# Optimization experiments

Hardware: AMD Instinct MI355X
Metric: run time of the kernel (lower is better)

Reference implementation:

```python
import jax, jax.numpy as jnp
from jax import lax
import numpy as np

B, T, L = 8, 24, 145
DHID, DFRAME, DEMB, DGCN, V = 1024, 2500, 128, 512, 1024
PF = 300
DINP = DHID + DFRAME + DEMB + DGCN   # 4164 = LSTM input size
DCONT = DHID + DINP                  # 5188 = cont_t size
FLAT = 64 * 7 * 7                    # 3136
BN_EPS = 1e-5
BN_INV = float(1.0 / np.sqrt(1.0 + BN_EPS))  # eval BN with running mean 0, var 1


def setup_inputs() -> dict:
    key = jax.random.key(0)
    ks = iter(jax.random.split(key, 48))
    rn = lambda *s: jax.random.normal(next(ks), s, jnp.float32)
    w = lambda *s: 0.02 * rn(*s)
    return dict(
        enc=rn(B, L, DHID),
        frames=rn(B, T, 512, 7, 7),
        gcn_embedding=rn(B, DGCN),
        h0=jnp.zeros((B, DHID), jnp.float32),
        c0=jnp.zeros((B, DHID), jnp.float32),
        conv1_w=w(256, 512), conv1_b=jnp.zeros((256,), jnp.float32),
        bn1_g=jnp.ones((256,), jnp.float32), bn1_b=jnp.zeros((256,), jnp.float32),
        conv2_w=w(64, 256), conv2_b=jnp.zeros((64,), jnp.float32),
        bn2_g=jnp.ones((64,), jnp.float32), bn2_b=jnp.zeros((64,), jnp.float32),
        fc_w=w(DFRAME, FLAT), fc_b=jnp.zeros((DFRAME,), jnp.float32),
        hfc_w=w(DHID, DHID), hfc_b=jnp.zeros((DHID,), jnp.float32),
        w_ih=w(4 * DHID, DINP), w_hh=w(4 * DHID, DHID),
        b_ih=jnp.zeros((4 * DHID,), jnp.float32), b_hh=jnp.zeros((4 * DHID,), jnp.float32),
        go=0.1 * rn(DEMB),
        emb_w=w(V, DEMB),
        actor_w=w(DEMB, DCONT), actor_b=jnp.zeros((DEMB,), jnp.float32),
        d1_w=w(FLAT, DCONT), d1_b=jnp.zeros((FLAT,), jnp.float32),
        dconv3_w=w(64, 32, 4, 4), dconv3_b=jnp.zeros((32,), jnp.float32),
        bnm2_g=jnp.ones((32,), jnp.float32), bnm2_b=jnp.zeros((32,), jnp.float32),
        dconv2_w=w(32, 16, 4, 4), dconv2_b=jnp.zeros((16,), jnp.float32),
        bnm1_g=jnp.ones((16,), jnp.float32), bnm1_b=jnp.zeros((16,), jnp.float32),
        dconv1_w=w(16, 1, 4, 4), dconv1_b=jnp.zeros((1,), jnp.float32),
    )


def _bn_eval(x, g, b):
    # BatchNorm2d in eval mode with running_mean=0, running_var=1
    return g[None, :, None, None] * (x * BN_INV) + b[None, :, None, None]


def _up2(x):
    # UpsamplingNearest2d(scale_factor=2)
    return jnp.repeat(jnp.repeat(x, 2, axis=2), 2, axis=3)


def _deconv(x, w, b):
    # ConvTranspose2d(k=4, s=2, p=1); torch weight layout (in, out, kH, kW)
    k = jnp.flip(w, (2, 3)).transpose(1, 0, 2, 3)  # -> (out, in, kH, kW)
    y = lax.conv_general_dilated(x, k, window_strides=(1, 1), padding=((2, 2), (2, 2)),
                                 lhs_dilation=(2, 2),
                                 dimension_numbers=('NCHW', 'OIHW', 'NCHW'))
    return y + b[None, :, None, None]


def reference(enc, frames, gcn_embedding, h0, c0,
              conv1_w, conv1_b, bn1_g, bn1_b, conv2_w, conv2_b, bn2_g, bn2_b, fc_w, fc_b,
              hfc_w, hfc_b, w_ih, w_hh, b_ih, b_hh, go, emb_w, actor_w, actor_b,
              d1_w, d1_b, dconv3_w, dconv3_b, bnm2_g, bnm2_b,
              dconv2_w, dconv2_b, bnm1_g, bnm1_b, dconv1_w, dconv1_b):

    def vis_encode(frame):  # [B,512,7,7] -> [B,DFRAME]
        x = jnp.einsum('bchw,oc->bohw', frame, conv1_w) + conv1_b[None, :, None, None]
        x = jax.nn.relu(_bn_eval(x, bn1_g, bn1_b))
        x = jnp.einsum('bchw,oc->bohw', x, conv2_w) + conv2_b[None, :, None, None]
        x = jax.nn.relu(_bn_eval(x, bn2_g, bn2_b))
        return x.reshape(-1, FLAT) @ fc_w.T + fc_b

    def mask_decode(cont):  # [B,DCONT] -> [B,1,300,300]
        x = jax.nn.relu(cont @ d1_w.T + d1_b).reshape(-1, 64, 7, 7)
        x = _deconv(_up2(x), dconv3_w, dconv3_b)          # 14 -> 28
        x = jax.nn.relu(_bn_eval(x, bnm2_g, bnm2_b))
        x = _deconv(_up2(x), dconv2_w, dconv2_b)          # 56 -> 112
        x = jax.nn.relu(_bn_eval(x, bnm1_g, bnm1_b))
        x = _deconv(x, dconv1_w, dconv1_b)                # 112 -> 224
        return jax.image.resize(x, (x.shape[0], 1, PF, PF), method='bilinear')

    def step(carry, frame_t):
        h, c, e_t = carry
        vis = vis_encode(frame_t)
        hq = h @ hfc_w.T + hfc_b
        score = jax.nn.softmax(jnp.einsum('bld,bd->bl', enc, hq), axis=1)  # [B,L]
        weighted = jnp.einsum('bl,bld->bd', score, enc)
        inp = jnp.concatenate([vis, weighted, e_t, gcn_embedding], axis=1)  # [B,DINP]
        gates = inp @ w_ih.T + b_ih + h @ w_hh.T + b_hh
        i, f, g, o = jnp.split(gates, 4, axis=1)
        c_new = jax.nn.sigmoid(f) * c + jax.nn.sigmoid(i) * jnp.tanh(g)
        h_new = jax.nn.sigmoid(o) * jnp.tanh(c_new)
        cont = jnp.concatenate([h_new, inp], axis=1)  # [B,DCONT]
        action = (cont @ actor_w.T + actor_b) @ emb_w.T  # [B,V]
        mask = mask_decode(cont)
        e_new = emb_w[jnp.argmax(action, axis=1)]  # greedy feed-back
        return (h_new, c_new, e_new), (action, mask, score[:, :, None])

    e0 = jnp.tile(go[None, :], (enc.shape[0], 1))
    (h_T, c_T, _), (actions, masks, attns) = lax.scan(
        step, (h0, c0, e0), jnp.swapaxes(frames, 0, 1))
    out_action = jnp.swapaxes(actions, 0, 1)   # [B,T,V]
    out_mask = jnp.swapaxes(masks, 0, 1)       # [B,T,1,300,300]
    out_attn = jnp.swapaxes(attns, 0, 1)       # [B,T,L,1]
    return (out_action, out_mask, out_attn, h_T, c_T)
```

## Files before the change

### kernel.cpp

```cpp
#include <hip/hip_runtime.h>
#include <cstdint>
#include <cstddef>

#define DEV __device__ __forceinline__
typedef short bf16x8 __attribute__((ext_vector_type(8)));
typedef float fl4 __attribute__((ext_vector_type(4)));
typedef float f32x4 __attribute__((ext_vector_type(4)));
typedef unsigned short u16;

#define BN_INV 0.9999950000375f

DEV float b2f(u16 u){ return __uint_as_float(((unsigned)u)<<16); }
DEV u16 f2b(float f){ unsigned u = __float_as_uint(f); unsigned r = (u + 0x7FFFu + ((u>>16)&1u))>>16; return (u16)r; }

DEV bf16x8 load8(const u16* p){ return *(const bf16x8*)p; }
DEV bf16x8 load8(const float* p){
  fl4 a = *(const fl4*)p; fl4 b = *(const fl4*)(p+4);
  bf16x8 r;
  r[0]=(short)f2b(a[0]); r[1]=(short)f2b(a[1]); r[2]=(short)f2b(a[2]); r[3]=(short)f2b(a[3]);
  r[4]=(short)f2b(b[0]); r[5]=(short)f2b(b[1]); r[6]=(short)f2b(b[2]); r[7]=(short)f2b(b[3]);
  return r;
}


__global__ __launch_bounds__(256) void k_pack_frames(const float* __restrict__ fr, u16* __restrict__ XT){
  int bt = blockIdx.x, tid = threadIdx.x;
  for (int e=0;e<128;e++){
    int flat = e*256 + tid;
    int p = flat>>9, c = flat&511;
    u16 v = 0;
    if (p < 49) v = f2b(fr[((size_t)bt*512 + c)*49 + p]);
    XT[((size_t)bt*64 + p)*512 + c] = v;
  }
}

__global__ __launch_bounds__(256) void k_pack_wseq(const float* __restrict__ w_ih, const float* __restrict__ w_hh,
                                                   u16* __restrict__ wseq){
  int r = blockIdx.x, tid = threadIdx.x;
  const float* wr = w_ih + (size_t)r*4164;
  for (int j=tid;j<2176;j+=256){
    float v = (j < 1024) ? w_hh[(size_t)r*1024 + j] : wr[2500 + (j-1024)];
    wseq[(size_t)r*2176 + j] = f2b(v);
  }
}

__global__ __launch_bounds__(256) void k_pack_dseq(const float* __restrict__ d1_w, const float* __restrict__ actor_w,
                                                   u16* __restrict__ dseq){
  int r = blockIdx.x, tid = threadIdx.x;
  const float* wr = (r < 3136) ? (d1_w + (size_t)r*5188) : (actor_w + (size_t)(r-3136)*5188);
  for (int j=tid;j<2176;j+=256){
    float v = (j < 1024) ? wr[j] : wr[3524 + (j-1024)];
    dseq[(size_t)r*2176 + j] = f2b(v);
  }
}

__global__ __launch_bounds__(256) void k_pack_wvg(const float* __restrict__ w_ih, u16* __restrict__ wvg, int rbase){
  int r = rbase + blockIdx.x, tid = threadIdx.x;
  const float* wr = w_ih + (size_t)r*4164;
  u16* dst = wvg + (size_t)blockIdx.x*3072;
  for (int j=tid;j<3072;j+=256){
    float v = 0.f;
    if (j < 2500) v = wr[j];
    else if (j < 3012) v = wr[3652 + (j-2500)];
    dst[j] = f2b(v);
  }
}

__global__ __launch_bounds__(256) void k_pack_dvg(const float* __restrict__ d1_w, const float* __restrict__ actor_w,
                                                  u16* __restrict__ dvg, int rbase){
  int r = rbase + blockIdx.x, tid = threadIdx.x;
  const float* wr = (r < 3136) ? (d1_w + (size_t)r*5188) : (actor_w + (size_t)(r-3136)*5188);
  u16* dst = dvg + (size_t)blockIdx.x*3072;
  for (int j=tid;j<3072;j+=256){
    float v = 0.f;
    if (j < 2500) v = wr[1024 + j];
    else if (j < 3012) v = wr[4676 + (j-2500)];
    dst[j] = f2b(v);
  }
}

__global__ __launch_bounds__(256) void k_hfcT(const float* __restrict__ hfc_w, u16* __restrict__ hfcT){
  int idx = blockIdx.x*256 + threadIdx.x;
  int k = idx>>10, o = idx&1023;
  hfcT[idx] = f2b(hfc_w[o*1024 + k]);
}

DEV u16 wt_map(const float* w, int n, int k, int CIN, int COUT){
  int o = n % COUT; int cls = n / COUT;
  if (cls >= 4) return 0;
  int py = cls>>1, px = cls&1;
  int i = k/9; int dd = k - i*9; int dy = dd/3, dx = dd - dy*3;
  if (i >= CIN) return 0;
  int ky = (py==0) ? (dy==0 ? 3 : (dy==1 ? 1 : -1)) : (dy==1 ? 2 : (dy==2 ? 0 : -1));
  int kx = (px==0) ? (dx==0 ? 3 : (dx==1 ? 1 : -1)) : (dx==1 ? 2 : (dx==2 ? 0 : -1));
  if (ky < 0 || kx < 0) return 0;
  return f2b(w[((i*COUT + o)*4 + ky)*4 + kx]);
}

__global__ __launch_bounds__(256) void k_misc(
  const float* b_ih, const float* b_hh, const float* d1_b, const float* actor_b,
  const float* emb_w, const float* h0, const float* c0,
  const float* dw3, const float* dw2, const float* dw1,
  float* bias_g, float* bias_da, u16* embT, float* hb0, float* cws,
  u16* Wt3, u16* Wt2, u16* Wt1)
{
  int blk = blockIdx.x, tid = threadIdx.x;
  if (blk < 16){ int i = blk*256+tid; if (i<4096) bias_g[i] = b_ih[i] + b_hh[i]; }
  else if (blk < 29){ int i = (blk-16)*256+tid; if (i<3264) bias_da[i] = (i<3136)? d1_b[i] : actor_b[i-3136]; }
  else if (blk < 541){ int i = (blk-29)*256+tid; int j = i>>10, v = i&1023; embT[i] = f2b(emb_w[v*128 + j]); }
  else if (blk < 573){ int i = (blk-541)*256+tid; if (i<8192){ hb0[i] = h0[i]; cws[i] = c0[i]; } }
  else if (blk < 574){ for (int i=tid;i<2560;i+=256){ int n=i/160, k=i-n*160; Wt1[i] = wt_map(dw1,n,k,16,1); } }
  else if (blk < 590){ for (int i=(blk-574)*256+tid; i<18432; i+=16*256){ int n=i/288, k=i-n*288; Wt2[i] = wt_map(dw2,n,k,32,16); } }
  else { for (int i=(blk-590)*256+tid; i<73728; i+=168*256){ int n=i/576, k=i-n*576; Wt3[i] = wt_map(dw3,n,k,64,32); } }
}

__global__ __launch_bounds__(256) void k_eb(const float* __restrict__ enc, const float* __restrict__ hfc_b, float* __restrict__ eb){
  int li = blockIdx.x*4 + (threadIdx.x>>6);
  int lane = threadIdx.x & 63;
  if (li >= 1160) return;
  const float* ep = enc + (size_t)li*1024;
  float a = 0.f;
  for (int k=lane;k<1024;k+=64) a += ep[k]*hfc_b[k];
  #pragma unroll
  for (int off=32; off; off>>=1) a += __shfl_xor(a, off);
  if (lane == 0) eb[li] = a;
}

__global__ __launch_bounds__(256) void k_vis_in(const u16* __restrict__ Y2, u16* __restrict__ vis_in){
  int bt = blockIdx.x, tid = threadIdx.x;
  for (int f=tid; f<3136; f+=256){
    int c = f/49, p = f - c*49;
    vis_in[(size_t)bt*3136 + f] = Y2[((size_t)bt*64 + p)*64 + c];
  }
}

__global__ __launch_bounds__(256) void k_xin(const u16* __restrict__ vis, const float* __restrict__ gcn, u16* __restrict__ xin2){
  int bt = blockIdx.x, tid = threadIdx.x, b = bt/24;
  for (int j=tid;j<3072;j+=256){
    u16 v = 0;
    if (j < 2500) v = vis[(size_t)bt*2500 + j];
    else if (j < 3012) v = f2b(gcn[b*512 + (j-2500)]);
    xin2[(size_t)bt*3072 + j] = v;
  }
}

template<int OUTB, int ACT, typename TA, typename TB>
__global__ __launch_bounds__(256) void gemm64(
  const TA* __restrict__ A, int lda, const TB* __restrict__ Bm, int ldb,
  void* __restrict__ Cv, int ldc, int M, int N, int K,
  const float* __restrict__ bias, const float* __restrict__ cb, const float* __restrict__ gg, const float* __restrict__ bb)
{
  __shared__ u16 sA[64*72];
  __shared__ u16 sB[64*72];
  int tid = threadIdx.x, lane = tid & 63, w = tid >> 6;
  int wm = w & 1, wn = w >> 1;
  int m0 = blockIdx.x*64, n0 = blockIdx.y*64;
  f32x4 acc[2][2];
  #pragma unroll
  for (int a=0;a<2;a++)
    #pragma unroll
    for (int b=0;b<2;b++){ acc[a][b][0]=0;acc[a][b][1]=0;acc[a][b][2]=0;acc[a][b][3]=0; }

  for (int k0=0;k0<K;k0+=64){
    #pragma unroll
    for (int j=0;j<2;j++){
      int c = tid + 256*j; int row = c>>3; int col = (c&7)*8;
      bf16x8 va = {0,0,0,0,0,0,0,0};
      int gm = m0 + row;
      if (gm < M) va = load8(A + (size_t)gm*lda + k0 + col);
      *(bf16x8*)(&sA[row*72 + col]) = va;
      bf16x8 vb = {0,0,0,0,0,0,0,0};
      int gn = n0 + row;
      if (gn < N) vb = load8(Bm + (size_t)gn*ldb + k0 + col);
      *(bf16x8*)(&sB[row*72 + col]) = vb;
    }
    __syncthreads();
    #pragma unroll
    for (int kk=0;kk<2;kk++){
      bf16x8 af[2], bfv[2];
      #pragma unroll
      for (int tm=0;tm<2;tm++) af[tm]  = *(const bf16x8*)(&sA[(wm*32+tm*16+(lane&15))*72 + kk*32 + (lane>>4)*8]);
      #pragma unroll
      for (int tn=0;tn<2;tn++) bfv[tn] = *(const bf16x8*)(&sB[(wn*32+tn*16+(lane&15))*72 + kk*32 + (lane>>4)*8]);
      #pragma unroll
      for (int tm=0;tm<2;tm++)
        #pragma unroll
        for (int tn=0;tn<2;tn++)
          acc[tm][tn] = __builtin_amdgcn_mfma_f32_16x16x32_bf16(af[tm], bfv[tn], acc[tm][tn], 0,0,0);
    }
    __syncthreads();
  }
  int ml = (lane>>4)*4, nl = lane&15;
  #pragma unroll
  for (int tm=0;tm<2;tm++)
    #pragma unroll
    for (int tn=0;tn<2;tn++)
      #pragma unroll
      for (int r=0;r<4;r++){
        int gm = m0 + wm*32 + tm*16 + ml + r;
        int gn = n0 + wn*32 + tn*16 + nl;
        if (gm < M && gn < N){
          float v = acc[tm][tn][r];
          if (ACT == 0){ if (bias) v += bias[gn]; }
          else { v = (v + cb[gn])*BN_INV*gg[gn] + bb[gn]; v = fmaxf(v, 0.f); }
          if (OUTB) ((u16*)Cv)[(size_t)gm*ldc + gn] = f2b(v);
          else      ((float*)Cv)[(size_t)gm*ldc + gn] = v;
        }
      }
}

template<int OUTB, typename TA, typename TB>
__global__ __launch_bounds__(64) void gemm16(
  const TA* __restrict__ A, int lda, const TB* __restrict__ Bm, int ldb,
  void* __restrict__ Cv, int ldc, int M, int N, int K, const float* __restrict__ bias)
{
  int lane = threadIdx.x;
  int m0 = blockIdx.x*16, n0 = blockIdx.y*16;
  int gm = m0 + (lane&15); if (gm > M-1) gm = M-1;
  int gn = n0 + (lane&15); if (gn > N-1) gn = N-1;
  const TA* ap = A  + (size_t)gm*lda + ((lane>>4)*8);
  const TB* bp = Bm + (size_t)gn*ldb + ((lane>>4)*8);
  f32x4 acc = {0,0,0,0};
  #pragma unroll 4
  for (int ks=0; ks<K; ks+=32){
    bf16x8 a = load8(ap + ks);
    bf16x8 b = load8(bp + ks);
    acc = __builtin_amdgcn_mfma_f32_16x16x32_bf16(a, b, acc, 0,0,0);
  }
  int nn = n0 + (lane&15);
  if (nn >= N) return;
  #pragma unroll
  for (int r=0;r<4;r++){
    int mm = m0 + (lane>>4)*4 + r;
    if (mm < M){
      float v = acc[r];
      if (bias) v += bias[nn];
      if (OUTB) ((u16*)Cv)[(size_t)mm*ldc + nn] = f2b(v);
      else      ((float*)Cv)[(size_t)mm*ldc + nn] = v;
    }
  }
}


__global__ __launch_bounds__(256) void p1_scores_action(
  const float* __restrict__ encH, const float* __restrict__ eb,
  const float* __restrict__ hcur, const float* __restrict__ cws,
  float* __restrict__ scores, const float* __restrict__ d1a_out,
  const u16* __restrict__ embT, float* __restrict__ out_act,
  float* __restrict__ cmv, int* __restrict__ cmi,
  float* __restrict__ out_h, float* __restrict__ out_c,
  u16* __restrict__ xb1, int t)
{
  __shared__ float shf[1024];
  __shared__ int shi[256];
  int blk = blockIdx.x, tid = threadIdx.x;
  if (blk < 40){
    if (t == 24) return;
    int b = blk/5, lc = blk - b*5;
    #pragma unroll
    for (int e=0;e<4;e++) shf[tid + 256*e] = hcur[b*1024 + tid + 256*e];
    __syncthreads();
    int w = tid>>6, lane = tid&63;
    for (int i=w;i<29;i+=4){
      int l = lc*29 + i;
      const float* ep = encH + (size_t)(b*145+l)*1024;
      float a = 0.f;
      for (int k=lane;k<1024;k+=64) a += ep[k]*shf[k];
      #pragma unroll
      for (int off=32; off; off>>=1) a += __shfl_xor(a, off);
      if (lane == 0) scores[b*145+l] = a + eb[b*145+l];
    }
  } else if (blk < 72){
    if (t == 0) return;
    int idx = blk-40; int b = idx>>2, vc = idx&3;
    if (tid < 128) shf[tid] = d1a_out[(size_t)(b*24 + t-1)*3264 + 3136 + tid];
    __syncthreads();
    int v = vc*256 + tid;
    float a = 0.f;
    for (int j=0;j<128;j++) a += shf[j]*b2f(embT[j*1024 + v]);
    out_act[(size_t)(b*24 + t-1)*1024 + v] = a;
    shf[256+tid] = a; shi[tid] = v;
    __syncthreads();
    for (int s=128; s; s>>=1){
      if (tid < s){
        float o = shf[256+tid+s]; int oi = shi[tid+s];
        float c = shf[256+tid];   int ci = shi[tid];
        if (o > c || (o == c && oi < ci)){ shf[256+tid] = o; shi[tid] = oi; }
      }
      __syncthreads();
    }
    if (tid == 0){ cmv[b*4+vc] = shf[256]; cmi[b*4+vc] = shi[0]; }
  } else {
    int b = blk-72;
    if (t == 24){
      #pragma unroll
      for (int e=0;e<4;e++){
        int k = tid + 256*e;
        out_h[b*1024+k] = hcur[b*1024+k];
        out_c[b*1024+k] = cws[b*1024+k];
      }
    } else {
      #pragma unroll
      for (int e=0;e<4;e++){
        int k = tid + 256*e;
        xb1[b*2176 + k] = f2b(hcur[b*1024+k]);
      }
    }
  }
}

__global__ __launch_bounds__(256) void p2_softmax_weighted(
  const float* __restrict__ scores, const float* __restrict__ enc,
  float* __restrict__ wgt, float* __restrict__ ecur,
  const float* __restrict__ cmv, const int* __restrict__ cmi,
  const float* __restrict__ emb_w, const float* __restrict__ go,
  float* __restrict__ out_attn, u16* __restrict__ xb1, u16* __restrict__ xb2, int t)
{
  int b = blockIdx.x >> 3, dc = blockIdx.x & 7, tid = threadIdx.x;
  __shared__ float s[145];
  __shared__ float mxs, invs;
  if (tid < 145) s[tid] = scores[b*145+tid];
  __syncthreads();
  if (tid < 64){
    float m = -1e30f;
    for (int i=tid;i<145;i+=64) m = fmaxf(m, s[i]);
    #pragma unroll
    for (int off=32; off; off>>=1) m = fmaxf(m, __shfl_xor(m, off));
    if (tid == 0) mxs = m;
  }
  __syncthreads();
  if (tid < 145) s[tid] = expf(s[tid]-mxs);
  __syncthreads();
  if (tid < 64){
    float sm = 0.f;
    for (int i=tid;i<145;i+=64) sm += s[i];
    #pragma unroll
    for (int off=32; off; off>>=1) sm += __shfl_xor(sm, off);
    if (tid == 0) invs = 1.f/sm;
  }
  __syncthreads();
  float inv = invs;
  if (tid < 128){
    int d = dc*128 + tid;
    float a = 0.f;
    for (int l=0;l<145;l++) a += s[l]*enc[(size_t)(b*145+l)*1024 + d];
    float wv = a*inv;
    wgt[b*1024+d] = wv;
    u16 wb = f2b(wv);
    xb1[b*2176 + 1024 + d] = wb;
    xb2[b*2176 + 1024 + d] = wb;
  } else {
    int i = tid-128;
    if (dc == 0){
      if (i < 145) out_attn[(size_t)(b*24+t)*145 + i] = s[i]*inv;
      int l2 = i + 128;
      if (l2 < 145) out_attn[(size_t)(b*24+t)*145 + l2] = s[l2]*inv;
    } else if (dc == 1){
      float ev;
      if (t == 0) ev = go[i];
      else {
        float bv = cmv[b*4]; int bi = cmi[b*4];
        #pragma unroll
        for (int c=1;c<4;c++){
          float v2 = cmv[b*4+c]; int i2 = cmi[b*4+c];
          if (v2 > bv || (v2 == bv && i2 < bi)){ bv = v2; bi = i2; }
        }
        ev = emb_w[bi*128 + i];
      }
      ecur[b*128+i] = ev;
      u16 eb16 = f2b(ev);
      xb1[b*2176 + 2048 + i] = eb16;
      xb2[b*2176 + 2048 + i] = eb16;
    }
  }
}

__global__ __launch_bounds__(64) void p3m(
  const u16* __restrict__ wseq, const u16* __restrict__ xb, float* __restrict__ gates4)
{
  int lane = threadIdx.x;
  int n = blockIdx.x*16 + (lane & 15);
  const u16* bp = wseq + (size_t)n*2176 + ((lane>>4)*8);
  const u16* ap = xb + (lane&7)*2176 + ((lane>>4)*8);
  f32x4 acc = {0,0,0,0};
  #pragma unroll 4
  for (int kk=0;kk<68;kk++){
    bf16x8 a = *(const bf16x8*)(ap + kk*32);
    bf16x8 b = *(const bf16x8*)(bp + kk*32);
    acc = __builtin_amdgcn_mfma_f32_16x16x32_bf16(a, b, acc, 0,0,0);
  }
  #pragma unroll
  for (int r=0;r<4;r++){
    int m = (lane>>4)*4 + r;
    if (m < 8) gates4[(size_t)m*4096 + n] = acc[r];
  }
}

__global__ __launch_bounds__(256) void p3l(
  const float* __restrict__ gates4, const float* __restrict__ gpre,
  float* __restrict__ hnew, float* __restrict__ cws, u16* __restrict__ xb2, int t)
{
  int idx = blockIdx.x*256 + threadIdx.x;
  int b = idx>>10, J = idx&1023;
  const float* gp = gpre + (size_t)(b*24+t)*4096;
  const float* gb = gates4 + (size_t)b*4096;
  float iv = gb[J]      + gp[J];
  float fv = gb[1024+J] + gp[1024+J];
  float gv = gb[2048+J] + gp[2048+J];
  float ov = gb[3072+J] + gp[3072+J];
  float ig = 1.f/(1.f+expf(-iv));
  float fg = 1.f/(1.f+expf(-fv));
  float gt = tanhf(gv);
  float og = 1.f/(1.f+expf(-ov));
  float cn = fg*cws[idx] + ig*gt;
  cws[idx] = cn;
  float hv = og*tanhf(cn);
  hnew[idx] = hv;
  xb2[b*2176 + J] = f2b(hv);
}

__global__ __launch_bounds__(64) void p4m(
  const u16* __restrict__ dseq, const u16* __restrict__ xb2,
  const float* __restrict__ dpre, float* __restrict__ dout, int t)
{
  int lane = threadIdx.x;
  int R = blockIdx.x*16 + (lane & 15);
  const u16* bp = dseq + (size_t)R*2176 + ((lane>>4)*8);
  const u16* ap = xb2 + (lane&7)*2176 + ((lane>>4)*8);
  f32x4 acc = {0,0,0,0};
  #pragma unroll 4
  for (int kk=0;kk<68;kk++){
    bf16x8 a = *(const bf16x8*)(ap + kk*32);
    bf16x8 b = *(const bf16x8*)(bp + kk*32);
    acc = __builtin_amdgcn_mfma_f32_16x16x32_bf16(a, b, acc, 0,0,0);
  }
  #pragma unroll
  for (int r=0;r<4;r++){
    int m = (lane>>4)*4 + r;
    if (m < 8){
      size_t row = (size_t)(m*24+t)*3264;
      dout[row + R] = acc[r] + dpre[row + R];
    }
  }
}


__global__ __launch_bounds__(256) void k_m0up(const float* __restrict__ d1a_out, float* __restrict__ m0up, int btbase){
  int cb = blockIdx.x;
  int idx = blockIdx.y*256 + threadIdx.x;
  int i = idx / 196; int rest = idx - i*196; int y = rest/14, x = rest - y*14;
  float v = d1a_out[(size_t)(btbase+cb)*3264 + i*49 + (y>>1)*7 + (x>>1)];
  m0up[(size_t)cb*12544 + idx] = fmaxf(v, 0.f);
}

DEV void stage_tile(u16* sAt, int ldk, int Ktot, int Kreal, const float* in_bt, int H, int p0, int tid){
  int m = tid & 15;
  int p = p0 + m;
  int u = p / H, v = p - u*H;
  bool pv = p < H*H;
  for (int k = tid>>4; k < Ktot; k += 16){
    float val = 0.f;
    if (k < Kreal && pv){
      int i = k/9; int dd = k - i*9; int dy = dd/3, dx = dd - dy*3;
      int uy = u + dy - 1, vx = v + dx - 1;
      if (uy >= 0 && uy < H && vx >= 0 && vx < H) val = in_bt[((size_t)i*H + uy)*H + vx];
    }
    sAt[m*ldk + k] = f2b(val);
  }
}

__global__ __launch_bounds__(256) void md3_deconv(const float* __restrict__ m0up, float* __restrict__ m1up,
  const u16* __restrict__ Wt3, const float* __restrict__ b3, const float* __restrict__ g3, const float* __restrict__ bb3)
{
  __shared__ u16 sAt[16*584];
  int tid = threadIdx.x, lane = tid&63, w = tid>>6;
  int cb = blockIdx.x;
  const float* in_bt = m0up + (size_t)cb*12544;
  float* out_bt = m1up + (size_t)cb*32*3136;
  int nt = blockIdx.y*4 + w;
  bf16x8 wc[18];
  #pragma unroll
  for (int ks=0;ks<18;ks++) wc[ks] = *(const bf16x8*)(Wt3 + (size_t)(nt*16 + (lane&15))*576 + ks*32 + (lane>>4)*8);
  int cls = nt>>1; int o = (nt&1)*16 + (lane&15);
  int py = cls>>1, px = cls&1;
  float cbv = b3[o], gv = g3[o], bbv = bb3[o];
  int mt = blockIdx.z;
  stage_tile(sAt, 584, 576, 576, in_bt, 14, mt*16, tid);
  __syncthreads();
  f32x4 acc = {0,0,0,0};
  #pragma unroll
  for (int ks=0;ks<18;ks++){
    bf16x8 a = *(const bf16x8*)(&sAt[(lane&15)*584 + ks*32 + (lane>>4)*8]);
    acc = __builtin_amdgcn_mfma_f32_16x16x32_bf16(a, wc[ks], acc, 0,0,0);
  }
  #pragma unroll
  for (int r=0;r<4;r++){
    int p = mt*16 + (lane>>4)*4 + r;
    if (p < 196){
      int u = p/14, v = p - (p/14)*14;
      float vv = fmaxf((acc[r] + cbv)*BN_INV*gv + bbv, 0.f);
      float* ob = out_bt + ((size_t)o*56 + 2*(2*u+py))*56 + 2*(2*v+px);
      ob[0]=vv; ob[1]=vv; ob[56]=vv; ob[57]=vv;
    }
  }
}

__global__ __launch_bounds__(256) void md2_deconv(const float* __restrict__ m1up, float* __restrict__ m2,
  const u16* __restrict__ Wt2, const float* __restrict__ b2, const float* __restrict__ g2, const float* __restrict__ bb2)
{
  __shared__ u16 sAt[16*296];
  int tid = threadIdx.x, lane = tid&63, w = tid>>6;
  int cb = blockIdx.x;
  const float* in_bt = m1up + (size_t)cb*32*3136;
  float* out_bt = m2 + (size_t)cb*16*12544;
  int nt = w;
  bf16x8 wc[9];
  #pragma unroll
  for (int ks=0;ks<9;ks++) wc[ks] = *(const bf16x8*)(Wt2 + (size_t)(nt*16 + (lane&15))*288 + ks*32 + (lane>>4)*8);
  int cls = nt; int o = lane&15;
  int py = cls>>1, px = cls&1;
  float cbv = b2[o], gv = g2[o], bbv = bb2[o];
  int mt = blockIdx.y;
  stage_tile(sAt, 296, 288, 288, in_bt, 56, mt*16, tid);
  __syncthreads();
  f32x4 acc = {0,0,0,0};
  #pragma unroll
  for (int ks=0;ks<9;ks++){
    bf16x8 a = *(const bf16x8*)(&sAt[(lane&15)*296 + ks*32 + (lane>>4)*8]);
    acc = __builtin_amdgcn_mfma_f32_16x16x32_bf16(a, wc[ks], acc, 0,0,0);
  }
  #pragma unroll
  for (int r=0;r<4;r++){
    int p = mt*16 + (lane>>4)*4 + r;
    if (p < 3136){
      int u = p/56, v = p - u*56;
      float vv = fmaxf((acc[r] + cbv)*BN_INV*gv + bbv, 0.f);
      out_bt[((size_t)o*112 + (2*u+py))*112 + (2*v+px)] = vv;
    }
  }
}

__global__ __launch_bounds__(256) void md1_direct(const float* __restrict__ m2, float* __restrict__ m3,
  const float* __restrict__ dw1, const float* __restrict__ b1)
{
  __shared__ float wl[256];
  int tid = threadIdx.x;
  wl[tid] = dw1[tid];
  __syncthreads();
  int cb = blockIdx.x;
  const float* in_bt = m2 + (size_t)cb*16*12544;
  float* out_bt = m3 + (size_t)cb*50176;
  int idx = blockIdx.y*256 + tid;
  int oy = idx/56, q = idx - oy*56;
  int ox0 = q*4;
  int iyA = (oy+1)>>1;  bool vA = iyA < 112;
  int iyB = iyA - 1;    bool vB = iyB >= 0;
  int kyA = (oy&1) ? 0 : 1;
  int kyB = kyA + 2;
  int xb = (ox0>>1) - 1;
  bool v0 = xb >= 0, v3 = (xb+3) < 112;
  int x0 = v0 ? xb : 0, x3 = v3 ? xb+3 : 111;
  float mA = vA ? 1.f : 0.f, mB = vB ? 1.f : 0.f;
  float mA0 = v0 ? mA : 0.f, mA3 = v3 ? mA : 0.f;
  float mB0 = v0 ? mB : 0.f, mB3 = v3 ? mB : 0.f;
  const float* rA = in_bt + (size_t)(vA ? iyA : 0)*112;
  const float* rB = in_bt + (size_t)(vB ? iyB : 0)*112;
  float acc0=0.f, acc1=0.f, acc2=0.f, acc3=0.f;
  #pragma unroll 4
  for (int i=0;i<16;i++){
    const float* cA = rA + i*12544;
    const float* cB = rB + i*12544;
    float a0 = cA[x0]*mA0, a1 = cA[xb+1]*mA, a2 = cA[xb+2]*mA, a3 = cA[x3]*mA3;
    float b0 = cB[x0]*mB0, b1v = cB[xb+1]*mB, b2 = cB[xb+2]*mB, b3 = cB[x3]*mB3;
    fl4 wA = *(const fl4*)(&wl[i*16 + kyA*4]);
    fl4 wB = *(const fl4*)(&wl[i*16 + kyB*4]);
    acc0 += a1*wA[1] + a0*wA[3] + b1v*wB[1] + b0*wB[3];
    acc1 += a2*wA[0] + a1*wA[2] + b2*wB[0] + b1v*wB[2];
    acc2 += a2*wA[1] + a1*wA[3] + b2*wB[1] + b1v*wB[3];
    acc3 += a3*wA[0] + a2*wA[2] + b3*wB[0] + b2*wB[2];
  }
  float bv = b1[0];
  fl4 o4 = {acc0+bv, acc1+bv, acc2+bv, acc3+bv};
  *(fl4*)(out_bt + (size_t)oy*224 + ox0) = o4;
}

__global__ __launch_bounds__(256) void k_resize(const float* __restrict__ m3, float* __restrict__ out_mask, int btbase){
  int cb = blockIdx.x;
  const float* in_bt = m3 + (size_t)cb*50176;
  int idx = blockIdx.y*256 + threadIdx.x;
  if (idx >= 90000) return;
  int oy = idx/300, ox = idx - oy*300;
  const float sc = 224.f/300.f;
  float sy = (oy+0.5f)*sc - 0.5f;
  float sx = (ox+0.5f)*sc - 0.5f;
  float fy = floorf(sy), fx = floorf(sx);
  float wy = sy-fy, wx = sx-fx;
  int y0 = (int)fy, x0 = (int)fx;
  int y0c = min(max(y0,0),223), y1c = min(max(y0+1,0),223);
  int x0c = min(max(x0,0),223), x1c = min(max(x0+1,0),223);
  float v00 = in_bt[y0c*224+x0c], v01 = in_bt[y0c*224+x1c];
  float v10 = in_bt[y1c*224+x0c], v11 = in_bt[y1c*224+x1c];
  float v = (1.f-wy)*((1.f-wx)*v00 + wx*v01) + wy*((1.f-wx)*v10 + wx*v11);
  out_mask[(size_t)(btbase+cb)*90000 + idx] = v;
}


extern "C" void kernel_launch(void* const* d_in, const int* in_sizes, int n_in,
                              void* d_out, int out_size, void* d_ws, size_t ws_size,
                              hipStream_t stream)
{
  const float* enc      = (const float*)d_in[0];
  const float* frames   = (const float*)d_in[1];
  const float* gcn      = (const float*)d_in[2];
  const float* h0       = (const float*)d_in[3];
  const float* c0       = (const float*)d_in[4];
  const float* conv1_w  = (const float*)d_in[5];
  const float* conv1_b  = (const float*)d_in[6];
  const float* bn1_g    = (const float*)d_in[7];
  const float* bn1_b    = (const float*)d_in[8];
  const float* conv2_w  = (const float*)d_in[9];
  const float* conv2_b  = (const float*)d_in[10];
  const float* bn2_g    = (const float*)d_in[11];
  const float* bn2_b    = (const float*)d_in[12];
  const float* fc_w     = (const float*)d_in[13];
  const float* fc_b     = (const float*)d_in[14];
  const float* hfc_w    = (const float*)d_in[15];
  const float* hfc_b    = (const float*)d_in[16];
  const float* w_ih     = (const float*)d_in[17];
  const float* w_hh     = (const float*)d_in[18];
  const float* b_ih     = (const float*)d_in[19];
  const float* b_hh     = (const float*)d_in[20];
  const float* go       = (const float*)d_in[21];
  const float* emb_w    = (const float*)d_in[22];
  const float* actor_w  = (const float*)d_in[23];
  const float* actor_b  = (const float*)d_in[24];
  const float* d1_w     = (const float*)d_in[25];
  const float* d1_b     = (const float*)d_in[26];
  const float* dconv3_w = (const float*)d_in[27];
  const float* dconv3_b = (const float*)d_in[28];
  const float* bnm2_g   = (const float*)d_in[29];
  const float* bnm2_b   = (const float*)d_in[30];
  const float* dconv2_w = (const float*)d_in[31];
  const float* dconv2_b = (const float*)d_in[32];
  const float* bnm1_g   = (const float*)d_in[33];
  const float* bnm1_b   = (const float*)d_in[34];
  const float* dconv1_w = (const float*)d_in[35];
  const float* dconv1_b = (const float*)d_in[36];
  (void)in_sizes; (void)n_in; (void)out_size;

  float* obase    = (float*)d_out;
  float* out_act  = obase;
  float* out_mask = obase + 196608;
  float* out_attn = obase + 17476608;
  float* out_h    = obase + 17504448;
  float* out_c    = obase + 17512640;

  char* ob = (char*)out_mask;
  size_t ooff = 0;
  auto oalloc = [&](size_t bytes)->char*{ char* p = ob + ooff; ooff = (ooff + bytes + 255) & ~(size_t)255; return p; };
  u16*   wseq      = (u16*)  oalloc(4096ULL*2176*2);
  u16*   dseq      = (u16*)  oalloc(3264ULL*2176*2);
  float* encH      = (float*)oalloc(1160ULL*1024*4);
  float* gates_pre = (float*)oalloc(192ULL*4096*4);
  float* d1a_pre   = (float*)oalloc(192ULL*3264*4);
  u16*   xin2      = (u16*)  oalloc(192ULL*3072*2);
  u16*   XT     = (u16*)oalloc(12288ULL*512*2);
  u16*   Y1     = (u16*)oalloc(12288ULL*256*2);
  u16*   Y2     = (u16*)oalloc(12288ULL*64*2);
  u16*   vis_in = (u16*)oalloc(192ULL*3136*2);
  u16*   vis    = (u16*)oalloc(192ULL*2500*2);
  u16*   wchunk = XT;

  char* wsb = (char*)d_ws;
  size_t off = 0;
  auto alloc = [&](size_t bytes)->char*{ char* p = wsb + off; off = (off + bytes + 255) & ~(size_t)255; return p; };
  float* d1a_out   = (float*)alloc(192ULL*3264*4);
  u16*   embT      = (u16*)  alloc(128ULL*1024*2);
  float* eb        = (float*)alloc(1160ULL*4);
  u16*   Wt3       = (u16*)  alloc(128ULL*576*2);
  u16*   Wt2       = (u16*)  alloc(64ULL*288*2);
  u16*   Wt1       = (u16*)  alloc(16ULL*160*2);
  float* hb        = (float*)alloc(2ULL*8192*4);
  float* c_ws      = (float*)alloc(8192ULL*4);
  float* e_cur     = (float*)alloc(8ULL*128*4);
  float* weighted  = (float*)alloc(8192ULL*4);
  float* scores_raw= (float*)alloc(8ULL*145*4);
  float* cmv       = (float*)alloc(32ULL*4);
  int*   cmi       = (int*)  alloc(32ULL*4);
  float* bias_g    = (float*)alloc(4096ULL*4);
  float* bias_da   = (float*)alloc(3264ULL*4);
  u16*   xb1       = (u16*)  alloc(8ULL*2176*2);
  u16*   xb2       = (u16*)  alloc(8ULL*2176*2);
  float* gates4    = (float*)alloc(8ULL*4096*4);
  size_t zbase = off;
  u16*   hfcT = (u16*)alloc(1024ULL*1024*2);

  const int cands[10] = {48,24,16,12,8,6,4,3,2,1};
  int C = 1;
  for (int i=0;i<10;i++){
    size_t need = zbase + (size_t)cands[i]*1455104ULL + 65536;
    if (need <= ws_size){ C = cands[i]; break; }
  }
  size_t mo = zbase;
  auto malloc_ = [&](size_t bytes)->char*{ char* p = wsb + mo; mo = (mo + bytes + 255) & ~(size_t)255; return p; };
  float* m0up = (float*)malloc_((size_t)C*12544*4);
  float* m1up = (float*)malloc_((size_t)C*32*3136*4);
  float* m2b  = (float*)malloc_((size_t)C*16*12544*4);
  float* m3b  = (float*)malloc_((size_t)C*50176*4);

  k_pack_frames<<<192, 256, 0, stream>>>(frames, XT);
  k_pack_wseq<<<4096, 256, 0, stream>>>(w_ih, w_hh, wseq);
  k_pack_dseq<<<3264, 256, 0, stream>>>(d1_w, actor_w, dseq);
  k_hfcT<<<4096, 256, 0, stream>>>(hfc_w, hfcT);
  k_misc<<<758, 256, 0, stream>>>(b_ih, b_hh, d1_b, actor_b, emb_w, h0, c0,
                                  dconv3_w, dconv2_w, dconv1_w,
                                  bias_g, bias_da, embT, hb, c_ws, Wt3, Wt2, Wt1);
  k_eb<<<290, 256, 0, stream>>>(enc, hfc_b, eb);

  gemm64<1,1><<<dim3(192,4), 256, 0, stream>>>(XT, 512, conv1_w, 512, Y1, 256, 12288, 256, 512, nullptr, conv1_b, bn1_g, bn1_b);
  gemm64<1,1><<<dim3(192,1), 256, 0, stream>>>(Y1, 256, conv2_w, 256, Y2, 64, 12288, 64, 256, nullptr, conv2_b, bn2_g, bn2_b);
  k_vis_in<<<192, 256, 0, stream>>>(Y2, vis_in);
  gemm16<1><<<dim3(12,157), 64, 0, stream>>>(vis_in, 3136, fc_w, 3136, vis, 2500, 192, 2500, 3136, fc_b);
  k_xin<<<192, 256, 0, stream>>>(vis, gcn, xin2);
  gemm16<0><<<dim3(73,64), 64, 0, stream>>>(enc, 1024, hfcT, 1024, encH, 1024, 1160, 1024, 1024, nullptr);

  for (int c=0;c<4;c++){
    k_pack_wvg<<<1024, 256, 0, stream>>>(w_ih, wchunk, c*1024);
    gemm16<0><<<dim3(12,64), 64, 0, stream>>>(xin2, 3072, wchunk, 3072, gates_pre + c*1024, 4096,
                                              192, 1024, 3072, bias_g + c*1024);
  }
  for (int c=0;c<3;c++){
    k_pack_dvg<<<1088, 256, 0, stream>>>(d1_w, actor_w, wchunk, c*1088);
    gemm16<0><<<dim3(12,68), 64, 0, stream>>>(xin2, 3072, wchunk, 3072, d1a_pre + c*1088, 3264,
                                              192, 1088, 3072, bias_da + c*1088);
  }

  for (int t=0; t<=24; t++){
    float* hcur = hb + (t&1)*8192;
    float* hnew = hb + ((t+1)&1)*8192;
    p1_scores_action<<<80, 256, 0, stream>>>(encH, eb, hcur, c_ws, scores_raw, d1a_out, embT,
                                             out_act, cmv, cmi, out_h, out_c, xb1, t);
    if (t == 24) break;
    p2_softmax_weighted<<<64, 256, 0, stream>>>(scores_raw, enc, weighted, e_cur, cmv, cmi, emb_w, go,
                                                out_attn, xb1, xb2, t);
    p3m<<<256, 64, 0, stream>>>(wseq, xb1, gates4);
    p3l<<<32, 256, 0, stream>>>(gates4, gates_pre, hnew, c_ws, xb2, t);
    p4m<<<204, 64, 0, stream>>>(dseq, xb2, d1a_pre, d1a_out, t);
  }

  for (int btbase=0; btbase<192; btbase+=C){
    k_m0up<<<dim3(C,49), 256, 0, stream>>>(d1a_out, m0up, btbase);
    md3_deconv<<<dim3(C,2,13), 256, 0, stream>>>(m0up, m1up, Wt3, dconv3_b, bnm2_g, bnm2_b);
    md2_deconv<<<dim3(C,196), 256, 0, stream>>>(m1up, m2b, Wt2, dconv2_b, bnm1_g, bnm1_b);
    md1_direct<<<dim3(C,49), 256, 0, stream>>>(m2b, m3b, dconv1_w, dconv1_b);
    k_resize<<<dim3(C,352), 256, 0, stream>>>(m3b, out_mask, btbase);
  }
}
```

Baseline: 3.286 ms.

## Fuse nearest upsampling into deconv staging and remap GEMM blocks across XCDs

After: 3.137 ms. 1.05x faster.

```diff
diff --git a/kernel.cpp b/kernel.cpp
--- a/kernel.cpp
+++ b/kernel.cpp
@@ -209,13 +209,22 @@
       }
 }
 
-template<int OUTB, typename TA, typename TB>
-__global__ __launch_bounds__(64) void gemm16(
+template<int OUTB, int NMAJOR, typename TA, typename TB>
+__global__ __launch_bounds__(64) void gemm16x(
   const TA* __restrict__ A, int lda, const TB* __restrict__ Bm, int ldb,
-  void* __restrict__ Cv, int ldc, int M, int N, int K, const float* __restrict__ bias)
-{
+  void* __restrict__ Cv, int ldc, int M, int N, int K, const float* __restrict__ bias,
+  int MT, int NT)
+{
+  int nb = gridDim.x;
+  int orig = blockIdx.x;
+  int q = nb >> 3, r = nb & 7;
+  int xcd = orig & 7, j = orig >> 3;
+  int wg = (xcd < r ? xcd*(q+1) : r*(q+1) + (xcd-r)*q) + j;
+  int bx, by;
+  if (NMAJOR){ bx = wg % MT; by = wg / MT; }
+  else       { by = wg % NT; bx = wg / NT; }
   int lane = threadIdx.x;
-  int m0 = blockIdx.x*16, n0 = blockIdx.y*16;
+  int m0 = bx*16, n0 = by*16;
   int gm = m0 + (lane&15); if (gm > M-1) gm = M-1;
   int gn = n0 + (lane&15); if (gn > N-1) gn = N-1;
   const TA* ap = A  + (size_t)gm*lda + ((lane>>4)*8);
@@ -230,10 +239,10 @@
   int nn = n0 + (lane&15);
   if (nn >= N) return;
   #pragma unroll
-  for (int r=0;r<4;r++){
-    int mm = m0 + (lane>>4)*4 + r;
+  for (int r2=0;r2<4;r2++){
+    int mm = m0 + (lane>>4)*4 + r2;
     if (mm < M){
-      float v = acc[r];
+      float v = acc[r2];
       if (bias) v += bias[nn];
       if (OUTB) ((u16*)Cv)[(size_t)mm*ldc + nn] = f2b(v);
       else      ((float*)Cv)[(size_t)mm*ldc + nn] = v;
@@ -445,12 +454,38 @@
 }
 
 
-__global__ __launch_bounds__(256) void k_m0up(const float* __restrict__ d1a_out, float* __restrict__ m0up, int btbase){
-  int cb = blockIdx.x;
-  int idx = blockIdx.y*256 + threadIdx.x;
-  int i = idx / 196; int rest = idx - i*196; int y = rest/14, x = rest - y*14;
-  float v = d1a_out[(size_t)(btbase+cb)*3264 + i*49 + (y>>1)*7 + (x>>1)];
-  m0up[(size_t)cb*12544 + idx] = fmaxf(v, 0.f);
+DEV void stage_tile3(u16* sAt, const float* __restrict__ d1a_bt, int p0, int tid){
+  int m = tid & 15;
+  int p = p0 + m;
+  int u = p / 14, v = p - u*14;
+  bool pv = p < 196;
+  for (int k = tid>>4; k < 576; k += 16){
+    float val = 0.f;
+    if (pv){
+      int i = k/9; int dd = k - i*9; int dy = dd/3, dx = dd - dy*3;
+      int uy = u + dy - 1, vx = v + dx - 1;
+      if (uy >= 0 && uy < 14 && vx >= 0 && vx < 14)
+        val = fmaxf(d1a_bt[i*49 + (uy>>1)*7 + (vx>>1)], 0.f);
+    }
+    sAt[m*584 + k] = f2b(val);
+  }
+}
+
+DEV void stage_tile2(u16* sAt, const float* __restrict__ m1c_bt, int p0, int tid){
+  int m = tid & 15;
+  int p = p0 + m;
+  int u = p / 56, v = p - u*56;
+  bool pv = p < 3136;
+  for (int k = tid>>4; k < 288; k += 16){
+    float val = 0.f;
+    if (pv){
+      int i = k/9; int dd = k - i*9; int dy = dd/3, dx = dd - dy*3;
+      int uy = u + dy - 1, vx = v + dx - 1;
+      if (uy >= 0 && uy < 56 && vx >= 0 && vx < 56)
+        val = m1c_bt[i*784 + (uy>>1)*28 + (vx>>1)];
+    }
+    sAt[m*296 + k] = f2b(val);
+  }
 }
 
 DEV void stage_tile(u16* sAt, int ldk, int Ktot, int Kreal, const float* in_bt, int H, int p0, int tid){
@@ -469,14 +504,14 @@
   }
 }
 
-__global__ __launch_bounds__(256) void md3_deconv(const float* __restrict__ m0up, float* __restrict__ m1up,
+__global__ __launch_bounds__(256) void md3_deconv(const float* __restrict__ d1a_out, int btbase, float* __restrict__ m1c,
   const u16* __restrict__ Wt3, const float* __restrict__ b3, const float* __restrict__ g3, const float* __restrict__ bb3)
 {
   __shared__ u16 sAt[16*584];
   int tid = threadIdx.x, lane = tid&63, w = tid>>6;
   int cb = blockIdx.x;
-  const float* in_bt = m0up + (size_t)cb*12544;
-  float* out_bt = m1up + (size_t)cb*32*3136;
+  const float* in_bt = d1a_out + (size_t)(btbase+cb)*3264;
+  float* out_bt = m1c + (size_t)cb*32*784;
   int nt = blockIdx.y*4 + w;
   bf16x8 wc[18];
   #pragma unroll
@@ -485,7 +520,7 @@
   int py = cls>>1, px = cls&1;
   float cbv = b3[o], gv = g3[o], bbv = bb3[o];
   int mt = blockIdx.z;
-  stage_tile(sAt, 584, 576, 576, in_bt, 14, mt*16, tid);
+  stage_tile3(sAt, in_bt, mt*16, tid);
   __syncthreads();
   f32x4 acc = {0,0,0,0};
   #pragma unroll
@@ -499,19 +534,18 @@
     if (p < 196){
       int u = p/14, v = p - (p/14)*14;
       float vv = fmaxf((acc[r] + cbv)*BN_INV*gv + bbv, 0.f);
-      float* ob = out_bt + ((size_t)o*56 + 2*(2*u+py))*56 + 2*(2*v+px);
-      ob[0]=vv; ob[1]=vv; ob[56]=vv; ob[57]=vv;
-    }
-  }
-}
-
-__global__ __launch_bounds__(256) void md2_deconv(const float* __restrict__ m1up, float* __restrict__ m2,
+      out_bt[((size_t)o*28 + (2*u+py))*28 + (2*v+px)] = vv;
+    }
+  }
+}
+
+__global__ __launch_bounds__(256) void md2_deconv(const float* __restrict__ m1c, float* __restrict__ m2,
   const u16* __restrict__ Wt2, const float* __restrict__ b2, const float* __restrict__ g2, const float* __restrict__ bb2)
 {
   __shared__ u16 sAt[16*296];
   int tid = threadIdx.x, lane = tid&63, w = tid>>6;
   int cb = blockIdx.x;
-  const float* in_bt = m1up + (size_t)cb*32*3136;
+  const float* in_bt = m1c + (size_t)cb*32*784;
   float* out_bt = m2 + (size_t)cb*16*12544;
   int nt = w;
   bf16x8 wc[9];
@@ -521,7 +555,7 @@
   int py = cls>>1, px = cls&1;
   float cbv = b2[o], gv = g2[o], bbv = bb2[o];
   int mt = blockIdx.y;
-  stage_tile(sAt, 296, 288, 288, in_bt, 56, mt*16, tid);
+  stage_tile2(sAt, in_bt, mt*16, tid);
   __syncthreads();
   f32x4 acc = {0,0,0,0};
   #pragma unroll
@@ -698,13 +732,12 @@
   const int cands[10] = {48,24,16,12,8,6,4,3,2,1};
   int C = 1;
   for (int i=0;i<10;i++){
-    size_t need = zbase + (size_t)cands[i]*1455104ULL + 65536;
+    size_t need = zbase + (size_t)cands[i]*1103872ULL + 65536;
     if (need <= ws_size){ C = cands[i]; break; }
   }
   size_t mo = zbase;
   auto malloc_ = [&](size_t bytes)->char*{ char* p = wsb + mo; mo = (mo + bytes + 255) & ~(size_t)255; return p; };
-  float* m0up = (float*)malloc_((size_t)C*12544*4);
-  float* m1up = (float*)malloc_((size_t)C*32*3136*4);
+  float* m1c  = (float*)malloc_((size_t)C*32*784*4);
   float* m2b  = (float*)malloc_((size_t)C*16*12544*4);
   float* m3b  = (float*)malloc_((size_t)C*50176*4);
 
@@ -720,19 +753,19 @@
   gemm64<1,1><<<dim3(192,4), 256, 0, stream>>>(XT, 512, conv1_w, 512, Y1, 256, 12288, 256, 512, nullptr, conv1_b, bn1_g, bn1_b);
   gemm64<1,1><<<dim3(192,1), 256, 0, stream>>>(Y1, 256, conv2_w, 256, Y2, 64, 12288, 64, 256, nullptr, conv2_b, bn2_g, bn2_b);
   k_vis_in<<<192, 256, 0, stream>>>(Y2, vis_in);
-  gemm16<1><<<dim3(12,157), 64, 0, stream>>>(vis_in, 3136, fc_w, 3136, vis, 2500, 192, 2500, 3136, fc_b);
+  gemm16x<1,1><<<12*157, 64, 0, stream>>>(vis_in, 3136, fc_w, 3136, vis, 2500, 192, 2500, 3136, fc_b, 12, 157);
   k_xin<<<192, 256, 0, stream>>>(vis, gcn, xin2);
-  gemm16<0><<<dim3(73,64), 64, 0, stream>>>(enc, 1024, hfcT, 1024, encH, 1024, 1160, 1024, 1024, nullptr);
-
-  for (int c=0;c<4;c++){
-    k_pack_wvg<<<1024, 256, 0, stream>>>(w_ih, wchunk, c*1024);
-    gemm16<0><<<dim3(12,64), 64, 0, stream>>>(xin2, 3072, wchunk, 3072, gates_pre + c*1024, 4096,
-                                              192, 1024, 3072, bias_g + c*1024);
-  }
-  for (int c=0;c<3;c++){
-    k_pack_dvg<<<1088, 256, 0, stream>>>(d1_w, actor_w, wchunk, c*1088);
-    gemm16<0><<<dim3(12,68), 64, 0, stream>>>(xin2, 3072, wchunk, 3072, d1a_pre + c*1088, 3264,
-                                              192, 1088, 3072, bias_da + c*1088);
+  gemm16x<0,0><<<73*64, 64, 0, stream>>>(enc, 1024, hfcT, 1024, encH, 1024, 1160, 1024, 1024, nullptr, 73, 64);
+
+  for (int c=0;c<2;c++){
+    k_pack_wvg<<<2048, 256, 0, stream>>>(w_ih, wchunk, c*2048);
+    gemm16x<0,1><<<12*128, 64, 0, stream>>>(xin2, 3072, wchunk, 3072, gates_pre + c*2048, 4096,
+                                            192, 2048, 3072, bias_g + c*2048, 12, 128);
+  }
+  for (int c=0;c<2;c++){
+    k_pack_dvg<<<1632, 256, 0, stream>>>(d1_w, actor_w, wchunk, c*1632);
+    gemm16x<0,1><<<12*102, 64, 0, stream>>>(xin2, 3072, wchunk, 3072, d1a_pre + c*1632, 3264,
+                                            192, 1632, 3072, bias_da + c*1632, 12, 102);
   }
 
   for (int t=0; t<=24; t++){
@@ -749,9 +782,8 @@
   }
 
   for (int btbase=0; btbase<192; btbase+=C){
-    k_m0up<<<dim3(C,49), 256, 0, stream>>>(d1a_out, m0up, btbase);
-    md3_deconv<<<dim3(C,2,13), 256, 0, stream>>>(m0up, m1up, Wt3, dconv3_b, bnm2_g, bnm2_b);
-    md2_deconv<<<dim3(C,196), 256, 0, stream>>>(m1up, m2b, Wt2, dconv2_b, bnm1_g, bnm1_b);
+    md3_deconv<<<dim3(C,2,13), 256, 0, stream>>>(d1a_out, btbase, m1c, Wt3, dconv3_b, bnm2_g, bnm2_b);
+    md2_deconv<<<dim3(C,196), 256, 0, stream>>>(m1c, m2b, Wt2, dconv2_b, bnm1_g, bnm1_b);
     md1_direct<<<dim3(C,49), 256, 0, stream>>>(m2b, m3b, dconv1_w, dconv1_b);
     k_resize<<<dim3(C,352), 256, 0, stream>>>(m3b, out_mask, btbase);
   }
```
